# Optimization experiments

Hardware: AMD Instinct MI355X
Metric: run time of the kernel (lower is better)

Reference implementation:

```python
import jax, jax.numpy as jnp
import numpy as np

N_NODES = 100000
N_EDGES = 1600000
NUM_GRAPHS = 256
EMB = 10
Z = 32
K = 64


def setup_inputs() -> dict:
    key = jax.random.key(0)
    ks = jax.random.split(key, 8)
    x = jax.random.randint(ks[0], (N_NODES,), 0, N_NODES)
    edge_index = jax.random.randint(ks[1], (2, N_EDGES), 0, N_NODES)
    edge_weight = jax.random.uniform(ks[2], (N_EDGES,), dtype=jnp.float32)
    batch = jnp.sort(jax.random.randint(ks[3], (N_NODES,), 0, NUM_GRAPHS))
    embed_table = jax.random.normal(ks[4], (N_NODES, EMB), dtype=jnp.float32)
    W_conv = jax.random.normal(ks[5], (EMB, Z), dtype=jnp.float32) / np.sqrt(EMB)
    b_conv = jax.random.normal(ks[6], (Z,), dtype=jnp.float32) * 0.01
    W_read = jax.random.normal(ks[7], (Z, K), dtype=jnp.float32) / np.sqrt(Z)
    return {"x": x, "edge_index": edge_index, "edge_weight": edge_weight,
            "batch": batch, "embed_table": embed_table, "W_conv": W_conv,
            "b_conv": b_conv, "W_read": W_read}


def reference(x, edge_index, edge_weight, batch, embed_table, W_conv, b_conv, W_read):
    n = x.shape[0]
    # Embedding lookup (squeeze is a no-op for 1-D index input)
    h = embed_table[x]                       # [N, 10]
    # GCNConv with improved=True: linear transform first (small EMB->Z)
    h = h @ W_conv                           # [N, Z]
    # gcn_norm: add self-loops with fill value 2.0 (improved)
    row, col = edge_index[0], edge_index[1]
    loop = jnp.arange(n)
    row_f = jnp.concatenate([row, loop])
    col_f = jnp.concatenate([col, loop])
    w_f = jnp.concatenate([edge_weight, jnp.full((n,), 2.0, edge_weight.dtype)])
    deg = jax.ops.segment_sum(w_f, col_f, num_segments=n)        # [N]
    d_inv_sqrt = jnp.where(deg > 0, jax.lax.rsqrt(jnp.where(deg > 0, deg, 1.0)), 0.0)
    norm = d_inv_sqrt[row_f] * w_f * d_inv_sqrt[col_f]           # [E+N]
    # gather-scale-scatter: out[col] += norm * h[row]
    msgs = h[row_f] * norm[:, None]                              # [E+N, Z]
    out = jax.ops.segment_sum(msgs, col_f, num_segments=n) + b_conv  # [N, Z]
    # global_mean_pool over batch assignment
    sums = jax.ops.segment_sum(out, batch, num_segments=NUM_GRAPHS)      # [G, Z]
    cnts = jax.ops.segment_sum(jnp.ones((n,), out.dtype), batch, num_segments=NUM_GRAPHS)
    pooled = sums / jnp.maximum(cnts, 1.0)[:, None]              # [G, Z]
    logits = pooled @ W_read                                     # [G, K]
    return (pooled, logits)
```

## Files before the change

### kernel.cpp

```cpp
#include <hip/hip_runtime.h>
#include <hip/hip_fp16.h>

#define GG 256
#define ZZDIM 32
#define KK 64
#define EMBD 10
#define BPG 4
#define SGRID (GG * BPG)
#define SLOTS 64
#define SPG (BPG * SLOTS)
#define MAXN 1024
#define CAP 16384



__global__ void lb_kernel(const int* __restrict__ batch, int* __restrict__ lb,
                          int* __restrict__ gcur, int n) {
    int g = threadIdx.x;
    int lo = 0, hi = n;
    while (lo < hi) {
        int mid = (lo + hi) >> 1;
        if (batch[mid] < g) lo = mid + 1; else hi = mid;
    }
    lb[g] = lo;
    if (g == 0) lb[GG] = n;
    gcur[g] = g * CAP;
}

__global__ void __launch_bounds__(512) bucket_kernel(
    const int* __restrict__ row, const int* __restrict__ col, const float* __restrict__ w,
    const int* __restrict__ batch, const int* __restrict__ lb,
    int* __restrict__ gcur, float2* __restrict__ rec, int e) {
    __shared__ int lcnt[GG], lres[GG], loff[GG], lbs[GG];
    for (int t = threadIdx.x; t < GG; t += 512) { lcnt[t] = 0; loff[t] = 0; lbs[t] = lb[t]; }
    __syncthreads();
    const long start = (long)blockIdx.x * 8192;
    int myg[16]; unsigned myp[16];
#pragma unroll
    for (int k = 0; k < 16; ++k) {
        long i = start + k * 512 + threadIdx.x;
        int g = -1;
        if (i < e) {
            int c = col[i];
            g = batch[c];
            myp[k] = ((unsigned)(c - lbs[g]) << 17) | (unsigned)row[i];
            atomicAdd(&lcnt[g], 1);
        }
        myg[k] = g;
    }
    __syncthreads();
    for (int t = threadIdx.x; t < GG; t += 512)
        if (lcnt[t]) lres[t] = atomicAdd(&gcur[t], lcnt[t]);
    __syncthreads();
#pragma unroll
    for (int k = 0; k < 16; ++k) {
        long i = start + k * 512 + threadIdx.x;
        if (i < e) {
            int g = myg[k];
            int slot = lres[g] + atomicAdd(&loff[g], 1);
            rec[slot] = make_float2(w[i], __int_as_float((int)myp[k]));
        }
    }
}

__global__ void degB_kernel(const float2* __restrict__ rec, const int* __restrict__ gcur,
                            const int* __restrict__ lb, float* __restrict__ dinv) {
    __shared__ float dl[MAXN];
    const int g = blockIdx.x;
    const int ns = lb[g], ne = lb[g + 1], sz = ne - ns;
    const long lo = (long)g * CAP;
    const long hi = gcur[g];
    if (sz <= MAXN) {
        for (int t = threadIdx.x; t < sz; t += 256) dl[t] = 2.0f;
        __syncthreads();
        for (long it = lo + threadIdx.x; it < hi; it += 256) {
            float2 r = rec[it];
            atomicAdd(&dl[(unsigned)__float_as_int(r.y) >> 17], r.x);
        }
        __syncthreads();
        for (int t = threadIdx.x; t < sz; t += 256) dinv[ns + t] = rsqrtf(dl[t]);
    } else {
        for (int t = threadIdx.x; t < sz; t += 256) dinv[ns + t] = 2.0f;
        __syncthreads();
        for (long it = lo + threadIdx.x; it < hi; it += 256) {
            float2 r = rec[it];
            atomicAdd(&dinv[ns + ((unsigned)__float_as_int(r.y) >> 17)], r.x);
        }
        __syncthreads();
        for (int t = threadIdx.x; t < sz; t += 256) dinv[ns + t] = rsqrtf(dinv[ns + t]);
    }
}

__global__ void hs_kernel(const int* __restrict__ x, const float* __restrict__ emb,
                          const float* __restrict__ Wc, const float* __restrict__ dinv,
                          __half2* __restrict__ hs16, int n) {
    int tid = blockIdx.x * blockDim.x + threadIdx.x;
    int i = tid >> 4, zp = tid & 15;
    if (i >= n) return;
    float d = dinv[i];
    int xi = x[i];
    const float* er = emb + (long)xi * EMBD;
    float a0 = 0.f, a1 = 0.f;
#pragma unroll
    for (int j = 0; j < EMBD; ++j) {
        float ej = er[j];
        a0 += ej * Wc[j * ZZDIM + 2 * zp];
        a1 += ej * Wc[j * ZZDIM + 2 * zp + 1];
    }
    hs16[(long)i * 16 + zp] = __floats2half2_rn(d * a0, d * a1);
}

__global__ void __launch_bounds__(512) scatter_kernel(
    const float2* __restrict__ rec, const int* __restrict__ gcur,
    const int* __restrict__ lb, const float* __restrict__ dinv,
    const uint2* __restrict__ hsq, float* __restrict__ partial) {
    __shared__ float dl[MAXN];
    const int z4   = threadIdx.x & 7;
    const int slot = threadIdx.x >> 3;
    const int g = blockIdx.x >> 2;
    const int q = blockIdx.x & 3;
    const int sg = q * SLOTS + slot;
    const int ns = lb[g], ne = lb[g + 1], sz = ne - ns;
    const bool inl = (sz <= MAXN);
    if (inl) for (int t = threadIdx.x; t < sz; t += 512) dl[t] = dinv[ns + t];
    __syncthreads();

    float4 acc = make_float4(0.f, 0.f, 0.f, 0.f);

#define GATHER4(pp) hsq[(long)((pp) & 0x1FFFFu) * 8 + z4]
#define ACCUM(c, v) do {                                              \
        float2 f0 = __half22float2(*(const __half2*)&(v).x);          \
        float2 f1 = __half22float2(*(const __half2*)&(v).y);          \
        acc.x = fmaf((c), f0.x, acc.x); acc.y = fmaf((c), f0.y, acc.y);\
        acc.z = fmaf((c), f1.x, acc.z); acc.w = fmaf((c), f1.y, acc.w);\
    } while (0)

    const long lo = (long)g * CAP;
    const long hi = gcur[g];
    long it = lo + sg;
    for (; it + 3L * SPG < hi; it += 4L * SPG) {
        float2 r0 = rec[it];
        float2 r1 = rec[it + SPG];
        float2 r2 = rec[it + 2L * SPG];
        float2 r3 = rec[it + 3L * SPG];
        unsigned p0 = (unsigned)__float_as_int(r0.y), p1 = (unsigned)__float_as_int(r1.y);
        unsigned p2 = (unsigned)__float_as_int(r2.y), p3 = (unsigned)__float_as_int(r3.y);
        uint2 v0 = GATHER4(p0);
        uint2 v1 = GATHER4(p1);
        uint2 v2 = GATHER4(p2);
        uint2 v3 = GATHER4(p3);
        float c0 = r0.x * (inl ? dl[p0 >> 17] : dinv[ns + (p0 >> 17)]);
        float c1 = r1.x * (inl ? dl[p1 >> 17] : dinv[ns + (p1 >> 17)]);
        float c2 = r2.x * (inl ? dl[p2 >> 17] : dinv[ns + (p2 >> 17)]);
        float c3 = r3.x * (inl ? dl[p3 >> 17] : dinv[ns + (p3 >> 17)]);
        ACCUM(c0, v0); ACCUM(c1, v1); ACCUM(c2, v2); ACCUM(c3, v3);
    }
    for (; it < hi; it += SPG) {
        float2 r = rec[it];
        unsigned p = (unsigned)__float_as_int(r.y);
        uint2 v = GATHER4(p);
        float c = r.x * (inl ? dl[p >> 17] : dinv[ns + (p >> 17)]);
        ACCUM(c, v);
    }

    for (long i = ns + sg; i < ne; i += SPG) {
        float c2v = 2.0f * (inl ? dl[i - ns] : dinv[i]);
        uint2 v = hsq[i * 8 + z4];
        ACCUM(c2v, v);
    }
#undef GATHER4
#undef ACCUM

    __shared__ float4 s[SLOTS][8];
    __shared__ float4 s2[8][8];
    s[slot][z4] = acc;
    __syncthreads();
    if (threadIdx.x < 64) {
        int j = threadIdx.x & 7, part = threadIdx.x >> 3;
        float4 a = make_float4(0.f, 0.f, 0.f, 0.f);
#pragma unroll
        for (int k = 0; k < 8; ++k) {
            float4 b = s[part * 8 + k][j];
            a.x += b.x; a.y += b.y; a.z += b.z; a.w += b.w;
        }
        s2[part][j] = a;
    }
    __syncthreads();
    if (threadIdx.x < 8) {
        int j = threadIdx.x;
        float4 a = make_float4(0.f, 0.f, 0.f, 0.f);
#pragma unroll
        for (int k = 0; k < 8; ++k) {
            float4 b = s2[k][j];
            a.x += b.x; a.y += b.y; a.z += b.z; a.w += b.w;
        }
        *(float4*)&partial[(long)blockIdx.x * ZZDIM + j * 4] = a;
    }
}

__global__ void finalize_kernel(const float* __restrict__ partial, const int* __restrict__ lb,
                                const float* __restrict__ bc, const float* __restrict__ Wr,
                                float* __restrict__ out) {
    int g = blockIdx.x;
    int t = threadIdx.x;
    __shared__ float p[ZZDIM];
    if (t < ZZDIM) {
        float a = 0.f;
#pragma unroll
        for (int q = 0; q < BPG; ++q) a += partial[(long)(g * BPG + q) * ZZDIM + t];
        float c = (float)(lb[g + 1] - lb[g]);
        float v = (c > 0.f) ? (bc[t] + a / c) : 0.f;
        out[g * ZZDIM + t] = v;
        p[t] = v;
    }
    __syncthreads();
    float a = 0.f;
#pragma unroll
    for (int zz = 0; zz < ZZDIM; ++zz) a += p[zz] * Wr[zz * KK + t];
    out[GG * ZZDIM + g * KK + t] = a;
}


extern "C" void kernel_launch(void* const* d_in, const int* in_sizes, int n_in,
                              void* d_out, int out_size, void* d_ws, size_t ws_size,
                              hipStream_t stream) {
    const int*   x     = (const int*)d_in[0];
    const int*   ei    = (const int*)d_in[1];
    const float* ew    = (const float*)d_in[2];
    const int*   batch = (const int*)d_in[3];
    const float* emb   = (const float*)d_in[4];
    const float* Wc    = (const float*)d_in[5];
    const float* bc    = (const float*)d_in[6];
    const float* Wr    = (const float*)d_in[7];
    float* out = (float*)d_out;

    const int n = in_sizes[0];
    const int e = in_sizes[2];

    float* ws   = (float*)d_ws;
    __half2* hs16 = (__half2*)ws;
    float* dinv = ws + 16L * n;
    int*  lb    = (int*)(ws + 17L * n);
    int*  gcur  = lb + GG + 1;
    long rbase = 17L * n + (2 * GG + 1);
    rbase = (rbase + 63) & ~63L;
    float2* rec = (float2*)(ws + rbase);
    long pbase = rbase + 2L * GG * CAP;
    pbase = (pbase + 63) & ~63L;
    float* partial = ws + pbase;

    lb_kernel<<<1, 256, 0, stream>>>(batch, lb, gcur, n);
    bucket_kernel<<<(e + 8191) / 8192, 512, 0, stream>>>(ei, ei + e, ew, batch, lb, gcur, rec, e);
    degB_kernel<<<GG, 256, 0, stream>>>(rec, gcur, lb, dinv);
    hs_kernel<<<(n * 16 + 255) / 256, 256, 0, stream>>>(x, emb, Wc, dinv, hs16, n);
    scatter_kernel<<<SGRID, 512, 0, stream>>>(rec, gcur, lb, dinv, (const uint2*)hs16, partial);
    finalize_kernel<<<GG, KK, 0, stream>>>(partial, lb, bc, Wr, out);
}
```

Measured before the change: 84.18 us.

## Fuse finalize into scatter with one block per graph, shrink bucket chunks

The scatter kernel now runs one 512-thread block per graph instead of four, and performs the mean-pool, bias and readout matmul itself, which removes the finalize kernel launch and the partial buffer round-trip. The bucket kernel processes 4096 edges per block instead of 8192, which doubles its grid and halves register arrays per thread. The trade-off is that the scatter grid drops to 256 blocks, so each block walks about four times more edges serially and the GPU may be underfilled during the main gather.

```diff
diff --git a/kernel.cpp b/kernel.cpp
--- a/kernel.cpp
+++ b/kernel.cpp
@@ -5,10 +5,7 @@
 #define ZZDIM 32
 #define KK 64
 #define EMBD 10
-#define BPG 4
-#define SGRID (GG * BPG)
 #define SLOTS 64
-#define SPG (BPG * SLOTS)
 #define MAXN 1024
 #define CAP 16384
 
@@ -32,12 +29,12 @@
     const int* __restrict__ batch, const int* __restrict__ lb,
     int* __restrict__ gcur, float2* __restrict__ rec, int e) {
     __shared__ int lcnt[GG], lres[GG], loff[GG], lbs[GG];
-    for (int t = threadIdx.x; t < GG; t += 512) { lcnt[t] = 0; loff[t] = 0; lbs[t] = lb[t]; }
-    __syncthreads();
-    const long start = (long)blockIdx.x * 8192;
-    int myg[16]; unsigned myp[16];
-#pragma unroll
-    for (int k = 0; k < 16; ++k) {
+    if (threadIdx.x < GG) { lcnt[threadIdx.x] = 0; loff[threadIdx.x] = 0; lbs[threadIdx.x] = lb[threadIdx.x]; }
+    __syncthreads();
+    const long start = (long)blockIdx.x * 4096;
+    int myg[8]; unsigned myp[8];
+#pragma unroll
+    for (int k = 0; k < 8; ++k) {
         long i = start + k * 512 + threadIdx.x;
         int g = -1;
         if (i < e) {
@@ -49,11 +46,11 @@
         myg[k] = g;
     }
     __syncthreads();
-    for (int t = threadIdx.x; t < GG; t += 512)
-        if (lcnt[t]) lres[t] = atomicAdd(&gcur[t], lcnt[t]);
-    __syncthreads();
-#pragma unroll
-    for (int k = 0; k < 16; ++k) {
+    if (threadIdx.x < GG && lcnt[threadIdx.x])
+        lres[threadIdx.x] = atomicAdd(&gcur[threadIdx.x], lcnt[threadIdx.x]);
+    __syncthreads();
+#pragma unroll
+    for (int k = 0; k < 8; ++k) {
         long i = start + k * 512 + threadIdx.x;
         if (i < e) {
             int g = myg[k];
@@ -113,13 +110,12 @@
 __global__ void __launch_bounds__(512) scatter_kernel(
     const float2* __restrict__ rec, const int* __restrict__ gcur,
     const int* __restrict__ lb, const float* __restrict__ dinv,
-    const uint2* __restrict__ hsq, float* __restrict__ partial) {
+    const uint2* __restrict__ hsq, const float* __restrict__ bc,
+    const float* __restrict__ Wr, float* __restrict__ out) {
     __shared__ float dl[MAXN];
     const int z4   = threadIdx.x & 7;
     const int slot = threadIdx.x >> 3;
-    const int g = blockIdx.x >> 2;
-    const int q = blockIdx.x & 3;
-    const int sg = q * SLOTS + slot;
+    const int g = blockIdx.x;
     const int ns = lb[g], ne = lb[g + 1], sz = ne - ns;
     const bool inl = (sz <= MAXN);
     if (inl) for (int t = threadIdx.x; t < sz; t += 512) dl[t] = dinv[ns + t];
@@ -137,12 +133,12 @@
 
     const long lo = (long)g * CAP;
     const long hi = gcur[g];
-    long it = lo + sg;
-    for (; it + 3L * SPG < hi; it += 4L * SPG) {
+    long it = lo + slot;
+    for (; it + 3L * SLOTS < hi; it += 4L * SLOTS) {
         float2 r0 = rec[it];
-        float2 r1 = rec[it + SPG];
-        float2 r2 = rec[it + 2L * SPG];
-        float2 r3 = rec[it + 3L * SPG];
+        float2 r1 = rec[it + SLOTS];
+        float2 r2 = rec[it + 2L * SLOTS];
+        float2 r3 = rec[it + 3L * SLOTS];
         unsigned p0 = (unsigned)__float_as_int(r0.y), p1 = (unsigned)__float_as_int(r1.y);
         unsigned p2 = (unsigned)__float_as_int(r2.y), p3 = (unsigned)__float_as_int(r3.y);
         uint2 v0 = GATHER4(p0);
@@ -155,7 +151,7 @@
         float c3 = r3.x * (inl ? dl[p3 >> 17] : dinv[ns + (p3 >> 17)]);
         ACCUM(c0, v0); ACCUM(c1, v1); ACCUM(c2, v2); ACCUM(c3, v3);
     }
-    for (; it < hi; it += SPG) {
+    for (; it < hi; it += SLOTS) {
         float2 r = rec[it];
         unsigned p = (unsigned)__float_as_int(r.y);
         uint2 v = GATHER4(p);
@@ -163,7 +159,7 @@
         ACCUM(c, v);
     }
 
-    for (long i = ns + sg; i < ne; i += SPG) {
+    for (long i = ns + slot; i < ne; i += SLOTS) {
         float c2v = 2.0f * (inl ? dl[i - ns] : dinv[i]);
         uint2 v = hsq[i * 8 + z4];
         ACCUM(c2v, v);
@@ -173,6 +169,7 @@
 
     __shared__ float4 s[SLOTS][8];
     __shared__ float4 s2[8][8];
+    __shared__ float p[ZZDIM];
     s[slot][z4] = acc;
     __syncthreads();
     if (threadIdx.x < 64) {
@@ -186,38 +183,27 @@
         s2[part][j] = a;
     }
     __syncthreads();
-    if (threadIdx.x < 8) {
-        int j = threadIdx.x;
-        float4 a = make_float4(0.f, 0.f, 0.f, 0.f);
+    if (threadIdx.x < ZZDIM) {
+        int t = threadIdx.x;
+        int j = t >> 2, comp = t & 3;
+        float a = 0.f;
 #pragma unroll
         for (int k = 0; k < 8; ++k) {
-            float4 b = s2[k][j];
-            a.x += b.x; a.y += b.y; a.z += b.z; a.w += b.w;
-        }
-        *(float4*)&partial[(long)blockIdx.x * ZZDIM + j * 4] = a;
-    }
-}
-
-__global__ void finalize_kernel(const float* __restrict__ partial, const int* __restrict__ lb,
-                                const float* __restrict__ bc, const float* __restrict__ Wr,
-                                float* __restrict__ out) {
-    int g = blockIdx.x;
-    int t = threadIdx.x;
-    __shared__ float p[ZZDIM];
-    if (t < ZZDIM) {
-        float a = 0.f;
-#pragma unroll
-        for (int q = 0; q < BPG; ++q) a += partial[(long)(g * BPG + q) * ZZDIM + t];
-        float c = (float)(lb[g + 1] - lb[g]);
-        float v = (c > 0.f) ? (bc[t] + a / c) : 0.f;
+            const float4 b = s2[k][j];
+            a += (comp == 0) ? b.x : (comp == 1) ? b.y : (comp == 2) ? b.z : b.w;
+        }
+        float v = (sz > 0) ? (bc[t] + a / (float)sz) : 0.f;
         out[g * ZZDIM + t] = v;
         p[t] = v;
     }
     __syncthreads();
-    float a = 0.f;
-#pragma unroll
-    for (int zz = 0; zz < ZZDIM; ++zz) a += p[zz] * Wr[zz * KK + t];
-    out[GG * ZZDIM + g * KK + t] = a;
+    if (threadIdx.x < KK) {
+        int t = threadIdx.x;
+        float a = 0.f;
+#pragma unroll
+        for (int zz = 0; zz < ZZDIM; ++zz) a += p[zz] * Wr[zz * KK + t];
+        out[GG * ZZDIM + g * KK + t] = a;
+    }
 }
 
 
@@ -245,14 +231,10 @@
     long rbase = 17L * n + (2 * GG + 1);
     rbase = (rbase + 63) & ~63L;
     float2* rec = (float2*)(ws + rbase);
-    long pbase = rbase + 2L * GG * CAP;
-    pbase = (pbase + 63) & ~63L;
-    float* partial = ws + pbase;
 
     lb_kernel<<<1, 256, 0, stream>>>(batch, lb, gcur, n);
-    bucket_kernel<<<(e + 8191) / 8192, 512, 0, stream>>>(ei, ei + e, ew, batch, lb, gcur, rec, e);
+    bucket_kernel<<<(e + 4095) / 4096, 512, 0, stream>>>(ei, ei + e, ew, batch, lb, gcur, rec, e);
     degB_kernel<<<GG, 256, 0, stream>>>(rec, gcur, lb, dinv);
     hs_kernel<<<(n * 16 + 255) / 256, 256, 0, stream>>>(x, emb, Wc, dinv, hs16, n);
-    scatter_kernel<<<SGRID, 512, 0, stream>>>(rec, gcur, lb, dinv, (const uint2*)hs16, partial);
-    finalize_kernel<<<GG, KK, 0, stream>>>(partial, lb, bc, Wr, out);
-}
+    scatter_kernel<<<GG, 512, 0, stream>>>(rec, gcur, lb, dinv, (const uint2*)hs16, bc, Wr, out);
+}
```

Result: slower. 89.87 us (+6.8%).
